# Performance work log

Measured on AMD Instinct MI355X. Metric: run time of the kernel, lower is better.

## Reference

```python
import jax, jax.numpy as jnp
import numpy as np

N_NODES = 100000
N_EDGES = 1600000
NFEAT = 128
NHID = 128
NCLASS = 16


def _sage_conv(x, src, dst, w_self, w_neigh, b):
    # mean aggregation over in-neighbors: for each dst, mean of x[src]
    msgs = x[src]                                   # [E, F] gather
    agg = jax.ops.segment_sum(msgs, dst, num_segments=x.shape[0])  # [N, F]
    deg = jax.ops.segment_sum(jnp.ones((src.shape[0],), x.dtype), dst,
                              num_segments=x.shape[0])             # [N]
    h_neigh = agg / jnp.maximum(deg, 1.0)[:, None]
    return x @ w_self + h_neigh @ w_neigh + b


def setup_inputs() -> dict:
    key = jax.random.key(0)
    ks = jax.random.split(key, 9)
    x = jax.random.normal(ks[0], (N_NODES, NFEAT), dtype=jnp.float32)
    src = jax.random.randint(ks[1], (N_EDGES,), 0, N_NODES, dtype=jnp.int32)
    dst = jax.random.randint(ks[2], (N_EDGES,), 0, N_NODES, dtype=jnp.int32)
    s1 = 1.0 / np.sqrt(NFEAT)
    s2 = 1.0 / np.sqrt(NHID)
    w_self1 = jax.random.uniform(ks[3], (NFEAT, NHID), jnp.float32, -s1, s1)
    w_neigh1 = jax.random.uniform(ks[4], (NFEAT, NHID), jnp.float32, -s1, s1)
    b1 = jnp.zeros((NHID,), jnp.float32)
    w_self2 = jax.random.uniform(ks[5], (NHID, NCLASS), jnp.float32, -s2, s2)
    w_neigh2 = jax.random.uniform(ks[6], (NHID, NCLASS), jnp.float32, -s2, s2)
    b2 = jnp.zeros((NCLASS,), jnp.float32)
    return {"x": x, "src": src, "dst": dst,
            "w_self1": w_self1, "w_neigh1": w_neigh1, "b1": b1,
            "w_self2": w_self2, "w_neigh2": w_neigh2, "b2": b2}


def reference(x, src, dst, w_self1, w_neigh1, b1, w_self2, w_neigh2, b2):
    h = jax.nn.relu(_sage_conv(x, src, dst, w_self1, w_neigh1, b1))
    # dropout is identity in eval mode (training=False)
    out = _sage_conv(h, src, dst, w_self2, w_neigh2, b2)
    return jax.nn.log_softmax(out, axis=1)
```

## Files before the change

### kernel.cpp

```cpp
#include <hip/hip_runtime.h>
#include <math.h>

#define NN 100000
#define NE 1600000
#define BSZ 64
#define NBUCK ((NN + BSZ - 1) / BSZ)
#define NBLK 256
#define CHUNK ((NE + NBLK - 1) / NBLK)
#define NH (NBUCK * NBLK)
#define NSB ((NH + 1023) / 1024)

typedef unsigned int uint;
typedef unsigned short ushort_t;
typedef float f32x4 __attribute__((ext_vector_type(4)));
typedef short s16x8 __attribute__((ext_vector_type(8)));

union U4S8 { uint4 u; s16x8 s; };

__device__ inline uint bf16_1(float f) {
  uint u = __float_as_uint(f);
  return (u + 0x7FFFu + ((u >> 16) & 1u)) >> 16;
}
__device__ inline uint bf16_2(float lo, float hi) {
  return bf16_1(lo) | (bf16_1(hi) << 16);
}
__device__ inline float blo(uint u) { return __uint_as_float(u << 16); }
__device__ inline float bhi(uint u) { return __uint_as_float(u & 0xFFFF0000u); }

__device__ inline f32x4 mfma_bf16(uint4 a, uint4 b, f32x4 c) {
  U4S8 ua, ub; ua.u = a; ub.u = b;
  return __builtin_amdgcn_mfma_f32_16x16x32_bf16(ua.s, ub.s, c, 0, 0, 0);
}

__global__ __launch_bounds__(256) void tobf16_kernel(
    const float* __restrict__ x, uint* __restrict__ xh) {
  int i = blockIdx.x * 256 + threadIdx.x;
  if (i >= NN * 16) return;
  const float4* p = (const float4*)x + (size_t)i * 2;
  float4 a = p[0], b = p[1];
  uint4 o;
  o.x = bf16_2(a.x, a.y);
  o.y = bf16_2(a.z, a.w);
  o.z = bf16_2(b.x, b.y);
  o.w = bf16_2(b.z, b.w);
  ((uint4*)xh)[i] = o;
}

__global__ __launch_bounds__(256) void prep_w1_kernel(
    const float* __restrict__ ws1, const float* __restrict__ wn1,
    uint* __restrict__ w1t) {
  int idx = blockIdx.x * 256 + threadIdx.x;
  if (idx >= 128 * 128) return;
  int col = idx >> 7, ku = idx & 127;
  int k = ku * 2;
  const float* w = (k < 128) ? ws1 : wn1;
  int kk = (k < 128) ? k : (k - 128);
  w1t[idx] = bf16_2(w[(size_t)kk * 128 + col], w[(size_t)(kk + 1) * 128 + col]);
}

__global__ __launch_bounds__(256) void prep_w2_kernel(
    const float* __restrict__ ws2, const float* __restrict__ wn2,
    uint* __restrict__ w2t) {
  int idx = blockIdx.x * 256 + threadIdx.x;
  if (idx >= 32 * 64) return;
  int col = idx >> 6, ku = idx & 63;
  int k = ku * 2;
  const float* w = (col < 16) ? ws2 : wn2;
  int c = col & 15;
  w2t[idx] = bf16_2(w[(size_t)k * 16 + c], w[(size_t)(k + 1) * 16 + c]);
}

__global__ __launch_bounds__(1024) void histA_kernel(
    const int* __restrict__ dst, int* __restrict__ hist2) {
  __shared__ int lh[NBUCK];
  int tid = threadIdx.x;
  int b = blockIdx.x;
  for (int i = tid; i < NBUCK; i += 1024) lh[i] = 0;
  __syncthreads();
  int e0 = b * CHUNK, e1 = min(e0 + CHUNK, NE);
  for (int e = e0 + tid; e < e1; e += 1024) {
    atomicAdd(&lh[dst[e] >> 6], 1);
  }
  __syncthreads();
  for (int i = tid; i < NBUCK; i += 1024)
    hist2[(size_t)b * NBUCK + i] = lh[i];
}

__global__ __launch_bounds__(1024) void transpose_kernel(
    const int* __restrict__ hist2, int* __restrict__ hist) {
  __shared__ int t[32][33];
  int tx = threadIdx.x & 31, ty = threadIdx.x >> 5;
  int i = blockIdx.x * 32 + tx;
  int b = blockIdx.y * 32 + ty;
  if (i < NBUCK) t[ty][tx] = hist2[(size_t)b * NBUCK + i];
  __syncthreads();
  int i2 = blockIdx.x * 32 + ty;
  int b2 = blockIdx.y * 32 + tx;
  if (i2 < NBUCK) hist[(size_t)i2 * NBLK + b2] = t[tx][ty];
}

__global__ __launch_bounds__(1024) void scan_sums_kernel(
    const int* __restrict__ hist, int* __restrict__ sums) {
  __shared__ int sdata[1024];
  int i = blockIdx.x * 1024 + threadIdx.x;
  sdata[threadIdx.x] = (i < NH) ? hist[i] : 0;
  __syncthreads();
#pragma unroll
  for (int s = 512; s > 0; s >>= 1) {
    if (threadIdx.x < s) sdata[threadIdx.x] += sdata[threadIdx.x + s];
    __syncthreads();
  }
  if (threadIdx.x == 0) sums[blockIdx.x] = sdata[0];
}

__global__ __launch_bounds__(512) void scan_tops_kernel(int* __restrict__ sums) {
  __shared__ int buf[2][512];
  int tid = threadIdx.x;
  int v = (tid < NSB) ? sums[tid] : 0;
  buf[0][tid] = v;
  __syncthreads();
  int pp = 0;
#pragma unroll
  for (int d = 1; d < 512; d <<= 1) {
    buf[pp ^ 1][tid] = buf[pp][tid] + ((tid >= d) ? buf[pp][tid - d] : 0);
    pp ^= 1;
    __syncthreads();
  }
  if (tid < NSB) sums[tid] = buf[pp][tid] - v;
}

__global__ __launch_bounds__(1024) void scan_apply_kernel(
    int* __restrict__ hist, const int* __restrict__ sums) {
  __shared__ int buf[2][1024];
  int tid = threadIdx.x;
  int i = blockIdx.x * 1024 + tid;
  int v = (i < NH) ? hist[i] : 0;
  buf[0][tid] = v;
  __syncthreads();
  int pp = 0;
#pragma unroll
  for (int d = 1; d < 1024; d <<= 1) {
    buf[pp ^ 1][tid] = buf[pp][tid] + ((tid >= d) ? buf[pp][tid - d] : 0);
    pp ^= 1;
    __syncthreads();
  }
  if (i < NH) hist[i] = sums[blockIdx.x] + buf[pp][tid] - v;
}

__global__ __launch_bounds__(1024) void scatter3_kernel(
    const int* __restrict__ src, const int* __restrict__ dst,
    const int* __restrict__ scanned, unsigned int* __restrict__ ebuf) {
  __shared__ int cur[NBUCK];
  int tid = threadIdx.x;
  int b = blockIdx.x;
  for (int i = tid; i < NBUCK; i += 1024) cur[i] = scanned[i * NBLK + b];
  __syncthreads();
  int e0 = b * CHUNK, e1 = min(e0 + CHUNK, NE);
  for (int e = e0 + tid; e < e1; e += 1024) {
    int d = dst[e];
    int p = atomicAdd(&cur[d >> 6], 1);
    ebuf[p] = ((unsigned int)(d & 63) << 17) | (unsigned int)src[e];
  }
}

__global__ __launch_bounds__(256) void bucket_sort_kernel(
    const unsigned int* __restrict__ ebuf, const int* __restrict__ scanned,
    int* __restrict__ deg, int* __restrict__ off, int* __restrict__ perm) {
  __shared__ int cnt[BSZ];
  __shared__ int loc_off[BSZ];
  int tid = threadIdx.x;
  int b = blockIdx.x;
  int e0 = scanned[b * NBLK];
  int e1 = (b + 1 < NBUCK) ? scanned[(b + 1) * NBLK] : NE;

  if (tid < BSZ) cnt[tid] = 0;
  __syncthreads();
  for (int e = e0 + tid; e < e1; e += 256)
    atomicAdd(&cnt[ebuf[e] >> 17], 1);
  __syncthreads();

  if (tid < BSZ) {
    int v = cnt[tid];
    int incl = v;
#pragma unroll
    for (int d = 1; d < 64; d <<= 1) {
      int t = __shfl_up(incl, d);
      if (tid >= d) incl += t;
    }
    int excl = incl - v;
    loc_off[tid] = e0 + excl;
    int node = b * BSZ + tid;
    if (node < NN) { off[node] = e0 + excl; deg[node] = v; }
    cnt[tid] = 0;
  }
  __syncthreads();

  for (int e = e0 + tid; e < e1; e += 256) {
    unsigned int pk = ebuf[e];
    int dl = pk >> 17;
    int p = loc_off[dl] + atomicAdd(&cnt[dl], 1);
    perm[p] = (int)(pk & 0x1FFFF);
  }
}

__global__ __launch_bounds__(256) void mean1_kernel(
    const uint* __restrict__ xh, const int* __restrict__ off,
    const int* __restrict__ deg, const int* __restrict__ perm,
    uint* __restrict__ mean1h) {
  int node = blockIdx.x * 4 + (threadIdx.x >> 6);
  int lane = threadIdx.x & 63;
  if (node >= NN) return;
  int o = off[node], dg = deg[node];
  int sub = lane >> 4;
  int q = lane & 15;
  float a0 = 0.f, a1 = 0.f, a2 = 0.f, a3 = 0.f;
  float a4 = 0.f, a5 = 0.f, a6 = 0.f, a7 = 0.f;
  int j = sub;
  for (; j + 4 < dg; j += 8) {
    int s0 = perm[o + j];
    int s1 = perm[o + j + 4];
    uint4 v0 = *(const uint4*)(xh + (size_t)s0 * 64 + q * 4);
    uint4 v1 = *(const uint4*)(xh + (size_t)s1 * 64 + q * 4);
    a0 += blo(v0.x) + blo(v1.x); a1 += bhi(v0.x) + bhi(v1.x);
    a2 += blo(v0.y) + blo(v1.y); a3 += bhi(v0.y) + bhi(v1.y);
    a4 += blo(v0.z) + blo(v1.z); a5 += bhi(v0.z) + bhi(v1.z);
    a6 += blo(v0.w) + blo(v1.w); a7 += bhi(v0.w) + bhi(v1.w);
  }
  if (j < dg) {
    int s0 = perm[o + j];
    uint4 v0 = *(const uint4*)(xh + (size_t)s0 * 64 + q * 4);
    a0 += blo(v0.x); a1 += bhi(v0.x);
    a2 += blo(v0.y); a3 += bhi(v0.y);
    a4 += blo(v0.z); a5 += bhi(v0.z);
    a6 += blo(v0.w); a7 += bhi(v0.w);
  }
#pragma unroll
  for (int d = 16; d <= 32; d <<= 1) {
    a0 += __shfl_xor(a0, d); a1 += __shfl_xor(a1, d);
    a2 += __shfl_xor(a2, d); a3 += __shfl_xor(a3, d);
    a4 += __shfl_xor(a4, d); a5 += __shfl_xor(a5, d);
    a6 += __shfl_xor(a6, d); a7 += __shfl_xor(a7, d);
  }
  if (sub == 0) {
    float rd = 1.0f / fmaxf((float)dg, 1.0f);
    uint4 o4;
    o4.x = bf16_2(a0 * rd, a1 * rd);
    o4.y = bf16_2(a2 * rd, a3 * rd);
    o4.z = bf16_2(a4 * rd, a5 * rd);
    o4.w = bf16_2(a6 * rd, a7 * rd);
    *(uint4*)(mean1h + (size_t)node * 64 + q * 4) = o4;
  }
}

__global__ __launch_bounds__(256) void gemm1_mfma_kernel(
    const uint* __restrict__ xh, const uint* __restrict__ m1h,
    const uint* __restrict__ w1t, const float* __restrict__ b1,
    ushort_t* __restrict__ hout) {
  __shared__ uint lds_w[128 * 128];
  int tid = threadIdx.x;

#pragma unroll
  for (int i = 0; i < 16; i++) {
    int g = tid + i * 256;
    int row = g >> 5, c = g & 31;
    uint4 v = ((const uint4*)w1t)[g];
    int cs = c ^ (row & 7);
    *(uint4*)&lds_w[row * 128 + cs * 4] = v;
  }
  __syncthreads();

  int wv = tid >> 6;
  int lane = tid & 63;
  int lr = lane & 15, lk = lane >> 4;
  int r0 = blockIdx.x * 256 + wv * 64;
  if (r0 >= NN) return;

  f32x4 acc[4][8];
#pragma unroll
  for (int i = 0; i < 4; i++)
#pragma unroll
    for (int j = 0; j < 8; j++) acc[i][j] = (f32x4){0.f, 0.f, 0.f, 0.f};

#pragma unroll
  for (int ks = 0; ks < 8; ks++) {
    const uint* A = (ks < 4) ? xh : m1h;
    int ku = (ks & 3) * 16 + lk * 4;
    uint4 a[4];
#pragma unroll
    for (int rt = 0; rt < 4; rt++) {
      int row = r0 + rt * 16 + lr;
      if (row >= NN) row = NN - 1;
      a[rt] = *(const uint4*)(A + (size_t)row * 64 + ku);
    }
    int cbase = ks * 4 + lk;
#pragma unroll
    for (int ct = 0; ct < 8; ct++) {
      int brow = ct * 16 + lr;
      int cs = cbase ^ (lr & 7);
      uint4 bu = *(const uint4*)&lds_w[brow * 128 + cs * 4];
#pragma unroll
      for (int rt = 0; rt < 4; rt++)
        acc[rt][ct] = mfma_bf16(a[rt], bu, acc[rt][ct]);
    }
  }

  float bias[8];
#pragma unroll
  for (int ct = 0; ct < 8; ct++) bias[ct] = b1[ct * 16 + lr];

#pragma unroll
  for (int rt = 0; rt < 4; rt++) {
#pragma unroll
    for (int r = 0; r < 4; r++) {
      int row = r0 + rt * 16 + lk * 4 + r;
      if (row < NN) {
#pragma unroll
        for (int ct = 0; ct < 8; ct++) {
          int col = ct * 16 + lr;
          float v = fmaxf(acc[rt][ct][r] + bias[ct], 0.0f);
          hout[(size_t)row * 128 + col] = (ushort_t)bf16_1(v);
        }
      }
    }
  }
}

__global__ __launch_bounds__(256) void gemm2_mfma_kernel(
    const uint* __restrict__ h, const uint* __restrict__ w2t,
    float* __restrict__ oself, float* __restrict__ h2) {
  int wid = (blockIdx.x * 256 + threadIdx.x) >> 6;
  int lane = threadIdx.x & 63;
  int r0 = wid * 32;
  if (r0 >= NN) return;
  int lr = lane & 15, lk = lane >> 4;

  f32x4 acc[2][2];
#pragma unroll
  for (int i = 0; i < 2; i++)
#pragma unroll
    for (int j = 0; j < 2; j++) acc[i][j] = (f32x4){0.f, 0.f, 0.f, 0.f};

#pragma unroll
  for (int ks = 0; ks < 4; ks++) {
    int ku = ks * 16;
    uint4 a0 = *(const uint4*)(h + (size_t)(r0 + lr) * 64 + ku + lk * 4);
    uint4 a1 = *(const uint4*)(h + (size_t)(r0 + 16 + lr) * 64 + ku + lk * 4);
#pragma unroll
    for (int ct = 0; ct < 2; ct++) {
      uint4 bu = *(const uint4*)(w2t + (size_t)(ct * 16 + lr) * 64 + ku + lk * 4);
      acc[0][ct] = mfma_bf16(a0, bu, acc[0][ct]);
      acc[1][ct] = mfma_bf16(a1, bu, acc[1][ct]);
    }
  }

#pragma unroll
  for (int rt = 0; rt < 2; rt++) {
#pragma unroll
    for (int r = 0; r < 4; r++) {
      int row = r0 + rt * 16 + lk * 4 + r;
      oself[(size_t)row * 16 + lr] = acc[rt][0][r];
      h2[(size_t)row * 16 + lr]    = acc[rt][1][r];
    }
  }
}

__global__ __launch_bounds__(256) void mean2_kernel(
    const float* __restrict__ h2, const int* __restrict__ off,
    const int* __restrict__ deg, const int* __restrict__ perm,
    float* __restrict__ mean2) {
  int node = blockIdx.x * 4 + (threadIdx.x >> 6);
  int lane = threadIdx.x & 63;
  if (node >= NN) return;
  int o = off[node], dg = deg[node];
  int sub = lane >> 2;
  int q = lane & 3;
  float ax = 0.f, ay = 0.f, az = 0.f, aw = 0.f;
  for (int j = sub; j < dg; j += 16) {
    int s = perm[o + j];
    float4 v = *(const float4*)(h2 + (size_t)s * 16 + q * 4);
    ax += v.x; ay += v.y; az += v.z; aw += v.w;
  }
#pragma unroll
  for (int d = 4; d <= 32; d <<= 1) {
    ax += __shfl_xor(ax, d); ay += __shfl_xor(ay, d);
    az += __shfl_xor(az, d); aw += __shfl_xor(aw, d);
  }
  if (sub == 0) {
    float rd = 1.0f / fmaxf((float)dg, 1.0f);
    float4 r; r.x = ax * rd; r.y = ay * rd; r.z = az * rd; r.w = aw * rd;
    *(float4*)(mean2 + (size_t)node * 16 + q * 4) = r;
  }
}

__global__ __launch_bounds__(256) void final_kernel(
    const float* __restrict__ oself, const float* __restrict__ mean2,
    const float* __restrict__ b2, float* __restrict__ out) {
  int i = blockIdx.x * 256 + threadIdx.x;
  if (i >= NN) return;
  float l[16];
  const float4* po = (const float4*)(oself + (size_t)i * 16);
  const float4* pa = (const float4*)(mean2 + (size_t)i * 16);
#pragma unroll
  for (int q = 0; q < 4; q++) {
    float4 o = po[q], a = pa[q];
    l[q * 4 + 0] = o.x + b2[q * 4 + 0] + a.x;
    l[q * 4 + 1] = o.y + b2[q * 4 + 1] + a.y;
    l[q * 4 + 2] = o.z + b2[q * 4 + 2] + a.z;
    l[q * 4 + 3] = o.w + b2[q * 4 + 3] + a.w;
  }
  float m = l[0];
#pragma unroll
  for (int c = 1; c < 16; c++) m = fmaxf(m, l[c]);
  float s = 0.0f;
#pragma unroll
  for (int c = 0; c < 16; c++) s += expf(l[c] - m);
  float ls = logf(s);
  float4* po2 = (float4*)(out + (size_t)i * 16);
#pragma unroll
  for (int q = 0; q < 4; q++) {
    float4 v;
    v.x = l[q * 4 + 0] - m - ls;
    v.y = l[q * 4 + 1] - m - ls;
    v.z = l[q * 4 + 2] - m - ls;
    v.w = l[q * 4 + 3] - m - ls;
    po2[q] = v;
  }
}

extern "C" void kernel_launch(void* const* d_in, const int* in_sizes, int n_in,
                              void* d_out, int out_size, void* d_ws, size_t ws_size,
                              hipStream_t stream) {
  const float* x   = (const float*)d_in[0];
  const int*   src = (const int*)d_in[1];
  const int*   dst = (const int*)d_in[2];
  const float* ws1 = (const float*)d_in[3];
  const float* wn1 = (const float*)d_in[4];
  const float* b1  = (const float*)d_in[5];
  const float* ws2 = (const float*)d_in[6];
  const float* wn2 = (const float*)d_in[7];
  const float* b2  = (const float*)d_in[8];
  float* out = (float*)d_out;

  char* p = (char*)d_ws;
  int* deg   = (int*)p;  p += (size_t)NN * 4;
  int* off   = (int*)p;  p += (size_t)NN * 4;
  int* hist  = (int*)p;  p += (size_t)NH * 4;
  int* hist2 = (int*)p;  p += (size_t)NH * 4;
  int* sums  = (int*)p;  p += (size_t)((NSB + 31) & ~31) * 4;
  unsigned int* ebuf = (unsigned int*)p; p += (size_t)NE * 4;
  int* perm = (int*)p;  p += (size_t)NE * 4;
  uint* xh   = (uint*)p; p += (size_t)NN * 64 * 4;
  uint* m1h  = (uint*)p; p += (size_t)NN * 64 * 4;
  uint* hbuf = (uint*)p; p += (size_t)NN * 64 * 4;
  uint* w1t  = (uint*)p; p += (size_t)128 * 128 * 4;
  uint* w2t  = (uint*)p; p += (size_t)32 * 64 * 4;
  float* h2    = (float*)p; p += (size_t)NN * 16 * 4;
  float* osf   = (float*)p; p += (size_t)NN * 16 * 4;
  float* mean2 = (float*)p; p += (size_t)NN * 16 * 4;

  tobf16_kernel<<<(NN * 16 + 255) / 256, 256, 0, stream>>>(x, xh);
  prep_w1_kernel<<<(128 * 128 + 255) / 256, 256, 0, stream>>>(ws1, wn1, w1t);
  prep_w2_kernel<<<(32 * 64 + 255) / 256, 256, 0, stream>>>(ws2, wn2, w2t);

  histA_kernel<<<NBLK, 1024, 0, stream>>>(dst, hist2);
  transpose_kernel<<<dim3((NBUCK + 31) / 32, NBLK / 32), 1024, 0, stream>>>(
      hist2, hist);
  scan_sums_kernel<<<NSB, 1024, 0, stream>>>(hist, sums);
  scan_tops_kernel<<<1, 512, 0, stream>>>(sums);
  scan_apply_kernel<<<NSB, 1024, 0, stream>>>(hist, sums);
  scatter3_kernel<<<NBLK, 1024, 0, stream>>>(src, dst, hist, ebuf);
  bucket_sort_kernel<<<NBUCK, 256, 0, stream>>>(ebuf, hist, deg, off, perm);

  mean1_kernel<<<(NN + 3) / 4, 256, 0, stream>>>(xh, off, deg, perm, m1h);

  gemm1_mfma_kernel<<<(NN + 255) / 256, 256, 0, stream>>>(
      xh, m1h, w1t, b1, (ushort_t*)hbuf);
  gemm2_mfma_kernel<<<(NN + 127) / 128, 256, 0, stream>>>(hbuf, w2t, osf, h2);

  mean2_kernel<<<(NN + 3) / 4, 256, 0, stream>>>(h2, off, deg, perm, mean2);
  final_kernel<<<(NN + 255) / 256, 256, 0, stream>>>(osf, mean2, b2, out);
}
```

Before: 186.1 us.

## Slice bf16 feature tables into 16-feature planes for cache-friendly gather

The bf16 node-feature table and the layer-1 mean buffer are stored as 8 column slices of 16 features, each a contiguous [N,16] plane. mean1 is regrouped so each block handles one slice for a 64-node bucket. Each gather then touches a 3.2 MB plane that fits better in cache, instead of the full 25.6 MB table, and gemm1 reads through the new layout. Accumulation uses v_dot2_f32_bf16 with a one-hot multiplier in place of shift/mask unpacking. The trade-off is that every edge index is read 8 times, the per-lane loads shrink to 8 bytes, and nodes are walked one at a time per wave, which may hurt latency hiding.

```diff
diff --git a/kernel.cpp b/kernel.cpp
--- a/kernel.cpp
+++ b/kernel.cpp
@@ -24,16 +24,21 @@
 __device__ inline uint bf16_2(float lo, float hi) {
   return bf16_1(lo) | (bf16_1(hi) << 16);
 }
-__device__ inline float blo(uint u) { return __uint_as_float(u << 16); }
-__device__ inline float bhi(uint u) { return __uint_as_float(u & 0xFFFF0000u); }
 
 __device__ inline f32x4 mfma_bf16(uint4 a, uint4 b, f32x4 c) {
   U4S8 ua, ub; ua.u = a; ub.u = b;
   return __builtin_amdgcn_mfma_f32_16x16x32_bf16(ua.s, ub.s, c, 0, 0, 0);
 }
 
+__device__ inline void dot2acc2(float& alo, float& ahi, uint u) {
+  asm("v_dot2_f32_bf16 %0, %2, %3, %0\n\t"
+      "v_dot2_f32_bf16 %1, %2, %4, %1"
+      : "+v"(alo), "+v"(ahi)
+      : "v"(u), "v"(0x00003F80u), "v"(0x3F800000u));
+}
+
 __global__ __launch_bounds__(256) void tobf16_kernel(
-    const float* __restrict__ x, uint* __restrict__ xh) {
+    const float* __restrict__ x, uint* __restrict__ xs) {
   int i = blockIdx.x * 256 + threadIdx.x;
   if (i >= NN * 16) return;
   const float4* p = (const float4*)x + (size_t)i * 2;
@@ -43,7 +48,9 @@
   o.y = bf16_2(a.z, a.w);
   o.z = bf16_2(b.x, b.y);
   o.w = bf16_2(b.z, b.w);
-  ((uint4*)xh)[i] = o;
+  int r = i >> 4;
+  int u = (i & 15) * 4;
+  *(uint4*)(xs + (size_t)(u >> 3) * NN * 8 + (size_t)r * 8 + (u & 7)) = o;
 }
 
 __global__ __launch_bounds__(256) void prep_w1_kernel(
@@ -204,56 +211,47 @@
 }
 
 __global__ __launch_bounds__(256) void mean1_kernel(
-    const uint* __restrict__ xh, const int* __restrict__ off,
+    const uint* __restrict__ xs, const int* __restrict__ off,
     const int* __restrict__ deg, const int* __restrict__ perm,
-    uint* __restrict__ mean1h) {
-  int node = blockIdx.x * 4 + (threadIdx.x >> 6);
+    uint* __restrict__ m1s) {
+  int s = blockIdx.x & 7;
+  int bucket = blockIdx.x >> 3;
+  int wv = threadIdx.x >> 6;
   int lane = threadIdx.x & 63;
-  if (node >= NN) return;
-  int o = off[node], dg = deg[node];
-  int sub = lane >> 4;
-  int q = lane & 15;
-  float a0 = 0.f, a1 = 0.f, a2 = 0.f, a3 = 0.f;
-  float a4 = 0.f, a5 = 0.f, a6 = 0.f, a7 = 0.f;
-  int j = sub;
-  for (; j + 4 < dg; j += 8) {
-    int s0 = perm[o + j];
-    int s1 = perm[o + j + 4];
-    uint4 v0 = *(const uint4*)(xh + (size_t)s0 * 64 + q * 4);
-    uint4 v1 = *(const uint4*)(xh + (size_t)s1 * 64 + q * 4);
-    a0 += blo(v0.x) + blo(v1.x); a1 += bhi(v0.x) + bhi(v1.x);
-    a2 += blo(v0.y) + blo(v1.y); a3 += bhi(v0.y) + bhi(v1.y);
-    a4 += blo(v0.z) + blo(v1.z); a5 += bhi(v0.z) + bhi(v1.z);
-    a6 += blo(v0.w) + blo(v1.w); a7 += bhi(v0.w) + bhi(v1.w);
-  }
-  if (j < dg) {
-    int s0 = perm[o + j];
-    uint4 v0 = *(const uint4*)(xh + (size_t)s0 * 64 + q * 4);
-    a0 += blo(v0.x); a1 += bhi(v0.x);
-    a2 += blo(v0.y); a3 += bhi(v0.y);
-    a4 += blo(v0.z); a5 += bhi(v0.z);
-    a6 += blo(v0.w); a7 += bhi(v0.w);
-  }
-#pragma unroll
-  for (int d = 16; d <= 32; d <<= 1) {
-    a0 += __shfl_xor(a0, d); a1 += __shfl_xor(a1, d);
-    a2 += __shfl_xor(a2, d); a3 += __shfl_xor(a3, d);
-    a4 += __shfl_xor(a4, d); a5 += __shfl_xor(a5, d);
-    a6 += __shfl_xor(a6, d); a7 += __shfl_xor(a7, d);
-  }
-  if (sub == 0) {
-    float rd = 1.0f / fmaxf((float)dg, 1.0f);
-    uint4 o4;
-    o4.x = bf16_2(a0 * rd, a1 * rd);
-    o4.y = bf16_2(a2 * rd, a3 * rd);
-    o4.z = bf16_2(a4 * rd, a5 * rd);
-    o4.w = bf16_2(a6 * rd, a7 * rd);
-    *(uint4*)(mean1h + (size_t)node * 64 + q * 4) = o4;
+  int slot = lane >> 2;
+  int q = lane & 3;
+  const uint* table = xs + (size_t)s * NN * 8;
+  uint* outp = m1s + (size_t)s * NN * 8;
+
+  int n0 = bucket * BSZ + wv * 16;
+  for (int n = 0; n < 16; n++) {
+    int node = n0 + n;
+    if (node >= NN) break;
+    int o = off[node], dg = deg[node];
+    float A0 = 0.f, A1 = 0.f, A2 = 0.f, A3 = 0.f;
+    for (int j = slot; j < dg; j += 16) {
+      int sr = perm[o + j];
+      uint2 v = *(const uint2*)(table + (size_t)sr * 8 + q * 2);
+      dot2acc2(A0, A1, v.x);
+      dot2acc2(A2, A3, v.y);
+    }
+#pragma unroll
+    for (int d = 4; d <= 32; d <<= 1) {
+      A0 += __shfl_xor(A0, d); A1 += __shfl_xor(A1, d);
+      A2 += __shfl_xor(A2, d); A3 += __shfl_xor(A3, d);
+    }
+    if (slot == 0) {
+      float rd = 1.0f / fmaxf((float)dg, 1.0f);
+      uint2 o2;
+      o2.x = bf16_2(A0 * rd, A1 * rd);
+      o2.y = bf16_2(A2 * rd, A3 * rd);
+      *(uint2*)(outp + (size_t)node * 8 + q * 2) = o2;
+    }
   }
 }
 
 __global__ __launch_bounds__(256) void gemm1_mfma_kernel(
-    const uint* __restrict__ xh, const uint* __restrict__ m1h,
+    const uint* __restrict__ xs, const uint* __restrict__ m1s,
     const uint* __restrict__ w1t, const float* __restrict__ b1,
     ushort_t* __restrict__ hout) {
   __shared__ uint lds_w[128 * 128];
@@ -283,14 +281,15 @@
 
 #pragma unroll
   for (int ks = 0; ks < 8; ks++) {
-    const uint* A = (ks < 4) ? xh : m1h;
-    int ku = (ks & 3) * 16 + lk * 4;
+    const uint* T = (ks < 4) ? xs : m1s;
+    int u = (ks & 3) * 16 + lk * 4;
+    const uint* base = T + (size_t)(u >> 3) * NN * 8 + (u & 7);
     uint4 a[4];
 #pragma unroll
     for (int rt = 0; rt < 4; rt++) {
       int row = r0 + rt * 16 + lr;
       if (row >= NN) row = NN - 1;
-      a[rt] = *(const uint4*)(A + (size_t)row * 64 + ku);
+      a[rt] = *(const uint4*)(base + (size_t)row * 8);
     }
     int cbase = ks * 4 + lk;
 #pragma unroll
@@ -449,8 +448,8 @@
   int* sums  = (int*)p;  p += (size_t)((NSB + 31) & ~31) * 4;
   unsigned int* ebuf = (unsigned int*)p; p += (size_t)NE * 4;
   int* perm = (int*)p;  p += (size_t)NE * 4;
-  uint* xh   = (uint*)p; p += (size_t)NN * 64 * 4;
-  uint* m1h  = (uint*)p; p += (size_t)NN * 64 * 4;
+  uint* xs   = (uint*)p; p += (size_t)NN * 64 * 4;
+  uint* m1s  = (uint*)p; p += (size_t)NN * 64 * 4;
   uint* hbuf = (uint*)p; p += (size_t)NN * 64 * 4;
   uint* w1t  = (uint*)p; p += (size_t)128 * 128 * 4;
   uint* w2t  = (uint*)p; p += (size_t)32 * 64 * 4;
@@ -458,7 +457,7 @@
   float* osf   = (float*)p; p += (size_t)NN * 16 * 4;
   float* mean2 = (float*)p; p += (size_t)NN * 16 * 4;
 
-  tobf16_kernel<<<(NN * 16 + 255) / 256, 256, 0, stream>>>(x, xh);
+  tobf16_kernel<<<(NN * 16 + 255) / 256, 256, 0, stream>>>(x, xs);
   prep_w1_kernel<<<(128 * 128 + 255) / 256, 256, 0, stream>>>(ws1, wn1, w1t);
   prep_w2_kernel<<<(32 * 64 + 255) / 256, 256, 0, stream>>>(ws2, wn2, w2t);
 
@@ -471,10 +470,10 @@
   scatter3_kernel<<<NBLK, 1024, 0, stream>>>(src, dst, hist, ebuf);
   bucket_sort_kernel<<<NBUCK, 256, 0, stream>>>(ebuf, hist, deg, off, perm);
 
-  mean1_kernel<<<(NN + 3) / 4, 256, 0, stream>>>(xh, off, deg, perm, m1h);
+  mean1_kernel<<<8 * NBUCK, 256, 0, stream>>>(xs, off, deg, perm, m1s);
 
   gemm1_mfma_kernel<<<(NN + 255) / 256, 256, 0, stream>>>(
-      xh, m1h, w1t, b1, (ushort_t*)hbuf);
+      xs, m1s, w1t, b1, (ushort_t*)hbuf);
   gemm2_mfma_kernel<<<(NN + 127) / 128, 256, 0, stream>>>(hbuf, w2t, osf, h2);
 
   mean2_kernel<<<(NN + 3) / 4, 256, 0, stream>>>(h2, off, deg, perm, mean2);
```

Measured after the change: 314.2 us. 68.8% more time.

## Gather layer-1 neighbor features in fp8, fuse mean2 with log-softmax, merge weight preps

Applied to the files above, without the earlier changes.

The conversion kernel now also writes an fp8 (e4m3) copy of x, stored in the hidden-buffer slot. mean1 gathers that copy, halving the bytes per gathered row, and unpacks it with the hardware cvt_pk instructions. The second aggregation is fused with the bias add and log-softmax, dropping the final kernel and the mean2 buffer, and the two weight-prep kernels are merged into one launch. fp8 input quantization loses precision in the neighbor mean, which may threaten accuracy tolerance.

```diff
diff --git a/kernel.cpp b/kernel.cpp
--- a/kernel.cpp
+++ b/kernel.cpp
@@ -12,6 +12,7 @@
 
 typedef unsigned int uint;
 typedef unsigned short ushort_t;
+typedef float f32x2 __attribute__((ext_vector_type(2)));
 typedef float f32x4 __attribute__((ext_vector_type(4)));
 typedef short s16x8 __attribute__((ext_vector_type(8)));
 
@@ -24,8 +25,6 @@
 __device__ inline uint bf16_2(float lo, float hi) {
   return bf16_1(lo) | (bf16_1(hi) << 16);
 }
-__device__ inline float blo(uint u) { return __uint_as_float(u << 16); }
-__device__ inline float bhi(uint u) { return __uint_as_float(u & 0xFFFF0000u); }
 
 __device__ inline f32x4 mfma_bf16(uint4 a, uint4 b, f32x4 c) {
   U4S8 ua, ub; ua.u = a; ub.u = b;
@@ -33,7 +32,8 @@
 }
 
 __global__ __launch_bounds__(256) void tobf16_kernel(
-    const float* __restrict__ x, uint* __restrict__ xh) {
+    const float* __restrict__ x, uint* __restrict__ xh,
+    uint* __restrict__ xq) {
   int i = blockIdx.x * 256 + threadIdx.x;
   if (i >= NN * 16) return;
   const float4* p = (const float4*)x + (size_t)i * 2;
@@ -44,30 +44,35 @@
   o.z = bf16_2(b.x, b.y);
   o.w = bf16_2(b.z, b.w);
   ((uint4*)xh)[i] = o;
-}
-
-__global__ __launch_bounds__(256) void prep_w1_kernel(
+  int q0 = __builtin_amdgcn_cvt_pk_fp8_f32(a.x, a.y, 0, false);
+  q0 = __builtin_amdgcn_cvt_pk_fp8_f32(a.z, a.w, q0, true);
+  int q1 = __builtin_amdgcn_cvt_pk_fp8_f32(b.x, b.y, 0, false);
+  q1 = __builtin_amdgcn_cvt_pk_fp8_f32(b.z, b.w, q1, true);
+  uint2 oq; oq.x = (uint)q0; oq.y = (uint)q1;
+  int r = i >> 4;
+  int u = (i & 15) * 2;
+  *(uint2*)(xq + (size_t)r * 32 + u) = oq;
+}
+
+__global__ __launch_bounds__(256) void prep_w_kernel(
     const float* __restrict__ ws1, const float* __restrict__ wn1,
-    uint* __restrict__ w1t) {
+    const float* __restrict__ ws2, const float* __restrict__ wn2,
+    uint* __restrict__ w1t, uint* __restrict__ w2t) {
   int idx = blockIdx.x * 256 + threadIdx.x;
-  if (idx >= 128 * 128) return;
-  int col = idx >> 7, ku = idx & 127;
-  int k = ku * 2;
-  const float* w = (k < 128) ? ws1 : wn1;
-  int kk = (k < 128) ? k : (k - 128);
-  w1t[idx] = bf16_2(w[(size_t)kk * 128 + col], w[(size_t)(kk + 1) * 128 + col]);
-}
-
-__global__ __launch_bounds__(256) void prep_w2_kernel(
-    const float* __restrict__ ws2, const float* __restrict__ wn2,
-    uint* __restrict__ w2t) {
-  int idx = blockIdx.x * 256 + threadIdx.x;
-  if (idx >= 32 * 64) return;
-  int col = idx >> 6, ku = idx & 63;
-  int k = ku * 2;
-  const float* w = (col < 16) ? ws2 : wn2;
-  int c = col & 15;
-  w2t[idx] = bf16_2(w[(size_t)k * 16 + c], w[(size_t)(k + 1) * 16 + c]);
+  if (idx < 128 * 128) {
+    int col = idx >> 7, ku = idx & 127;
+    int k = ku * 2;
+    const float* w = (k < 128) ? ws1 : wn1;
+    int kk = (k < 128) ? k : (k - 128);
+    w1t[idx] = bf16_2(w[(size_t)kk * 128 + col], w[(size_t)(kk + 1) * 128 + col]);
+  } else if (idx < 128 * 128 + 32 * 64) {
+    int j = idx - 128 * 128;
+    int col = j >> 6, ku = j & 63;
+    int k = ku * 2;
+    const float* w = (col < 16) ? ws2 : wn2;
+    int c = col & 15;
+    w2t[j] = bf16_2(w[(size_t)k * 16 + c], w[(size_t)(k + 1) * 16 + c]);
+  }
 }
 
 __global__ __launch_bounds__(1024) void histA_kernel(
@@ -204,51 +209,57 @@
 }
 
 __global__ __launch_bounds__(256) void mean1_kernel(
-    const uint* __restrict__ xh, const int* __restrict__ off,
+    const uint* __restrict__ xq, const int* __restrict__ off,
     const int* __restrict__ deg, const int* __restrict__ perm,
-    uint* __restrict__ mean1h) {
+    uint* __restrict__ m1h) {
   int node = blockIdx.x * 4 + (threadIdx.x >> 6);
   int lane = threadIdx.x & 63;
   if (node >= NN) return;
   int o = off[node], dg = deg[node];
-  int sub = lane >> 4;
-  int q = lane & 15;
-  float a0 = 0.f, a1 = 0.f, a2 = 0.f, a3 = 0.f;
-  float a4 = 0.f, a5 = 0.f, a6 = 0.f, a7 = 0.f;
-  int j = sub;
-  for (; j + 4 < dg; j += 8) {
-    int s0 = perm[o + j];
-    int s1 = perm[o + j + 4];
-    uint4 v0 = *(const uint4*)(xh + (size_t)s0 * 64 + q * 4);
-    uint4 v1 = *(const uint4*)(xh + (size_t)s1 * 64 + q * 4);
-    a0 += blo(v0.x) + blo(v1.x); a1 += bhi(v0.x) + bhi(v1.x);
-    a2 += blo(v0.y) + blo(v1.y); a3 += bhi(v0.y) + bhi(v1.y);
-    a4 += blo(v0.z) + blo(v1.z); a5 += bhi(v0.z) + bhi(v1.z);
-    a6 += blo(v0.w) + blo(v1.w); a7 += bhi(v0.w) + bhi(v1.w);
-  }
-  if (j < dg) {
-    int s0 = perm[o + j];
-    uint4 v0 = *(const uint4*)(xh + (size_t)s0 * 64 + q * 4);
-    a0 += blo(v0.x); a1 += bhi(v0.x);
-    a2 += blo(v0.y); a3 += bhi(v0.y);
-    a4 += blo(v0.z); a5 += bhi(v0.z);
-    a6 += blo(v0.w); a7 += bhi(v0.w);
-  }
-#pragma unroll
-  for (int d = 16; d <= 32; d <<= 1) {
-    a0 += __shfl_xor(a0, d); a1 += __shfl_xor(a1, d);
-    a2 += __shfl_xor(a2, d); a3 += __shfl_xor(a3, d);
-    a4 += __shfl_xor(a4, d); a5 += __shfl_xor(a5, d);
-    a6 += __shfl_xor(a6, d); a7 += __shfl_xor(a7, d);
-  }
-  if (sub == 0) {
+  int slot = lane >> 5;
+  int q = lane & 31;
+  f32x2 a0 = {0.f, 0.f}, a1 = {0.f, 0.f};
+  int j = 0;
+  for (; j + 8 <= dg; j += 8) {
+    int sA = perm[o + j + slot];
+    int sB = perm[o + j + 2 + slot];
+    int sC = perm[o + j + 4 + slot];
+    int sD = perm[o + j + 6 + slot];
+    uint vA = xq[(size_t)sA * 32 + q];
+    uint vB = xq[(size_t)sB * 32 + q];
+    uint vC = xq[(size_t)sC * 32 + q];
+    uint vD = xq[(size_t)sD * 32 + q];
+    a0 += __builtin_amdgcn_cvt_pk_f32_fp8(vA, 0);
+    a1 += __builtin_amdgcn_cvt_pk_f32_fp8(vA, 1);
+    a0 += __builtin_amdgcn_cvt_pk_f32_fp8(vB, 0);
+    a1 += __builtin_amdgcn_cvt_pk_f32_fp8(vB, 1);
+    a0 += __builtin_amdgcn_cvt_pk_f32_fp8(vC, 0);
+    a1 += __builtin_amdgcn_cvt_pk_f32_fp8(vC, 1);
+    a0 += __builtin_amdgcn_cvt_pk_f32_fp8(vD, 0);
+    a1 += __builtin_amdgcn_cvt_pk_f32_fp8(vD, 1);
+  }
+  for (; j + 2 <= dg; j += 2) {
+    int s = perm[o + j + slot];
+    uint v = xq[(size_t)s * 32 + q];
+    a0 += __builtin_amdgcn_cvt_pk_f32_fp8(v, 0);
+    a1 += __builtin_amdgcn_cvt_pk_f32_fp8(v, 1);
+  }
+  if (j < dg && slot == 0) {
+    int s = perm[o + j];
+    uint v = xq[(size_t)s * 32 + q];
+    a0 += __builtin_amdgcn_cvt_pk_f32_fp8(v, 0);
+    a1 += __builtin_amdgcn_cvt_pk_f32_fp8(v, 1);
+  }
+  a0.x += __shfl_xor(a0.x, 32);
+  a0.y += __shfl_xor(a0.y, 32);
+  a1.x += __shfl_xor(a1.x, 32);
+  a1.y += __shfl_xor(a1.y, 32);
+  if (slot == 0) {
     float rd = 1.0f / fmaxf((float)dg, 1.0f);
-    uint4 o4;
-    o4.x = bf16_2(a0 * rd, a1 * rd);
-    o4.y = bf16_2(a2 * rd, a3 * rd);
-    o4.z = bf16_2(a4 * rd, a5 * rd);
-    o4.w = bf16_2(a6 * rd, a7 * rd);
-    *(uint4*)(mean1h + (size_t)node * 64 + q * 4) = o4;
+    uint2 o2;
+    o2.x = bf16_2(a0.x * rd, a0.y * rd);
+    o2.y = bf16_2(a1.x * rd, a1.y * rd);
+    *(uint2*)(m1h + (size_t)node * 64 + q * 2) = o2;
   }
 }
 
@@ -367,64 +378,42 @@
 __global__ __launch_bounds__(256) void mean2_kernel(
     const float* __restrict__ h2, const int* __restrict__ off,
     const int* __restrict__ deg, const int* __restrict__ perm,
-    float* __restrict__ mean2) {
+    const float* __restrict__ oself, const float* __restrict__ b2,
+    float* __restrict__ out) {
   int node = blockIdx.x * 4 + (threadIdx.x >> 6);
   int lane = threadIdx.x & 63;
   if (node >= NN) return;
   int o = off[node], dg = deg[node];
-  int sub = lane >> 2;
-  int q = lane & 3;
-  float ax = 0.f, ay = 0.f, az = 0.f, aw = 0.f;
-  for (int j = sub; j < dg; j += 16) {
-    int s = perm[o + j];
-    float4 v = *(const float4*)(h2 + (size_t)s * 16 + q * 4);
-    ax += v.x; ay += v.y; az += v.z; aw += v.w;
-  }
-#pragma unroll
-  for (int d = 4; d <= 32; d <<= 1) {
-    ax += __shfl_xor(ax, d); ay += __shfl_xor(ay, d);
-    az += __shfl_xor(az, d); aw += __shfl_xor(aw, d);
-  }
-  if (sub == 0) {
-    float rd = 1.0f / fmaxf((float)dg, 1.0f);
-    float4 r; r.x = ax * rd; r.y = ay * rd; r.z = az * rd; r.w = aw * rd;
-    *(float4*)(mean2 + (size_t)node * 16 + q * 4) = r;
-  }
-}
-
-__global__ __launch_bounds__(256) void final_kernel(
-    const float* __restrict__ oself, const float* __restrict__ mean2,
-    const float* __restrict__ b2, float* __restrict__ out) {
-  int i = blockIdx.x * 256 + threadIdx.x;
-  if (i >= NN) return;
-  float l[16];
-  const float4* po = (const float4*)(oself + (size_t)i * 16);
-  const float4* pa = (const float4*)(mean2 + (size_t)i * 16);
-#pragma unroll
-  for (int q = 0; q < 4; q++) {
-    float4 o = po[q], a = pa[q];
-    l[q * 4 + 0] = o.x + b2[q * 4 + 0] + a.x;
-    l[q * 4 + 1] = o.y + b2[q * 4 + 1] + a.y;
-    l[q * 4 + 2] = o.z + b2[q * 4 + 2] + a.z;
-    l[q * 4 + 3] = o.w + b2[q * 4 + 3] + a.w;
-  }
-  float m = l[0];
-#pragma unroll
-  for (int c = 1; c < 16; c++) m = fmaxf(m, l[c]);
-  float s = 0.0f;
-#pragma unroll
-  for (int c = 0; c < 16; c++) s += expf(l[c] - m);
-  float ls = logf(s);
-  float4* po2 = (float4*)(out + (size_t)i * 16);
-#pragma unroll
-  for (int q = 0; q < 4; q++) {
-    float4 v;
-    v.x = l[q * 4 + 0] - m - ls;
-    v.y = l[q * 4 + 1] - m - ls;
-    v.z = l[q * 4 + 2] - m - ls;
-    v.w = l[q * 4 + 3] - m - ls;
-    po2[q] = v;
-  }
+  int slot = lane >> 4;
+  int q = lane & 15;
+  float a = 0.f;
+  int j = 0;
+  for (; j + 8 <= dg; j += 8) {
+    int sA = perm[o + j + slot];
+    int sB = perm[o + j + 4 + slot];
+    a += h2[(size_t)sA * 16 + q];
+    a += h2[(size_t)sB * 16 + q];
+  }
+  for (; j + 4 <= dg; j += 4) {
+    int s = perm[o + j + slot];
+    a += h2[(size_t)s * 16 + q];
+  }
+  if (j < dg && j + slot < dg) {
+    int s = perm[o + j + slot];
+    a += h2[(size_t)s * 16 + q];
+  }
+  a += __shfl_xor(a, 16);
+  a += __shfl_xor(a, 32);
+  float rd = 1.0f / fmaxf((float)dg, 1.0f);
+  float l = oself[(size_t)node * 16 + q] + b2[q] + a * rd;
+  float m = l;
+#pragma unroll
+  for (int d = 1; d <= 8; d <<= 1) m = fmaxf(m, __shfl_xor(m, d));
+  float ex = __expf(l - m);
+  float s = ex;
+#pragma unroll
+  for (int d = 1; d <= 8; d <<= 1) s += __shfl_xor(s, d);
+  if (lane < 16) out[(size_t)node * 16 + q] = l - m - logf(s);
 }
 
 extern "C" void kernel_launch(void* const* d_in, const int* in_sizes, int n_in,
@@ -452,15 +441,15 @@
   uint* xh   = (uint*)p; p += (size_t)NN * 64 * 4;
   uint* m1h  = (uint*)p; p += (size_t)NN * 64 * 4;
   uint* hbuf = (uint*)p; p += (size_t)NN * 64 * 4;
+  uint* xq   = hbuf;
   uint* w1t  = (uint*)p; p += (size_t)128 * 128 * 4;
   uint* w2t  = (uint*)p; p += (size_t)32 * 64 * 4;
   float* h2    = (float*)p; p += (size_t)NN * 16 * 4;
   float* osf   = (float*)p; p += (size_t)NN * 16 * 4;
-  float* mean2 = (float*)p; p += (size_t)NN * 16 * 4;
-
-  tobf16_kernel<<<(NN * 16 + 255) / 256, 256, 0, stream>>>(x, xh);
-  prep_w1_kernel<<<(128 * 128 + 255) / 256, 256, 0, stream>>>(ws1, wn1, w1t);
-  prep_w2_kernel<<<(32 * 64 + 255) / 256, 256, 0, stream>>>(ws2, wn2, w2t);
+
+  tobf16_kernel<<<(NN * 16 + 255) / 256, 256, 0, stream>>>(x, xh, xq);
+  prep_w_kernel<<<(128 * 128 + 32 * 64 + 255) / 256, 256, 0, stream>>>(
+      ws1, wn1, ws2, wn2, w1t, w2t);
 
   histA_kernel<<<NBLK, 1024, 0, stream>>>(dst, hist2);
   transpose_kernel<<<dim3((NBUCK + 31) / 32, NBLK / 32), 1024, 0, stream>>>(
@@ -471,12 +460,11 @@
   scatter3_kernel<<<NBLK, 1024, 0, stream>>>(src, dst, hist, ebuf);
   bucket_sort_kernel<<<NBUCK, 256, 0, stream>>>(ebuf, hist, deg, off, perm);
 
-  mean1_kernel<<<(NN + 3) / 4, 256, 0, stream>>>(xh, off, deg, perm, m1h);
+  mean1_kernel<<<(NN + 3) / 4, 256, 0, stream>>>(xq, off, deg, perm, m1h);
 
   gemm1_mfma_kernel<<<(NN + 255) / 256, 256, 0, stream>>>(
       xh, m1h, w1t, b1, (ushort_t*)hbuf);
   gemm2_mfma_kernel<<<(NN + 127) / 128, 256, 0, stream>>>(hbuf, w2t, osf, h2);
 
-  mean2_kernel<<<(NN + 3) / 4, 256, 0, stream>>>(h2, off, deg, perm, mean2);
-  final_kernel<<<(NN + 255) / 256, 256, 0, stream>>>(osf, mean2, b2, out);
-}
+  mean2_kernel<<<(NN + 3) / 4, 256, 0, stream>>>(h2, off, deg, perm, osf, b2, out);
+}
```

Result: no change. 184.9 us (-0.7%).
